# Kernel optimization log

Measured on AMD Instinct MI355X. Metric: run time of the kernel, lower is better.

Reference implementation:

```python
import jax, jax.numpy as jnp
import numpy as np

N, D, K, P, A = 16384, 256, 32, 64, 5
H, KD, NPT, FACT = 8, 32, 8, 2
RBF_BINS, RBF_MAX, REL_CLIP = 16, 10.0, 32


def _norm(v, eps=1e-6):
    return v * jax.lax.rsqrt(jnp.square(v).sum(-1, keepdims=True) + eps)


def extract_frames(pos):
    # pos: [N, A, 3]; backbone atoms 0=N, 1=CA, 2=C (Gram-Schmidt AF-style frame)
    n, ca, c = pos[:, 0], pos[:, 1], pos[:, 2]
    e1 = _norm(c - ca)
    u = n - ca
    e2 = _norm(u - (u * e1).sum(-1, keepdims=True) * e1)
    e3 = jnp.cross(e1, e2)
    R = jnp.stack([e1, e2, e3], axis=-1)  # [N,3,3], columns = frame axes
    t = ca
    local = jnp.einsum('nji,naj->nai', R, pos - t[:, None])  # R^T (p - t)
    return R, t, local


def distance_rbf(d):
    centers = jnp.linspace(0.0, RBF_MAX, RBF_BINS)
    sigma = RBF_MAX / RBF_BINS
    return jnp.exp(-jnp.square((d[..., None] - centers) / sigma))


def layer_norm(x, scale, offset, eps=1e-5):
    mu = x.mean(-1, keepdims=True)
    var = jnp.square(x - mu).mean(-1, keepdims=True)
    return (x - mu) * jax.lax.rsqrt(var + eps) * scale + offset


def setup_inputs() -> dict:
    key = jax.random.key(0)
    ks = jax.random.split(key, 20)
    f32 = jnp.float32
    rnd = lambda i, shape, s=0.02: jax.random.normal(ks[i], shape, f32) * s
    inp = {}
    inp['local'] = jax.random.normal(ks[0], (N, D), f32)
    inp['pos'] = jax.random.normal(ks[1], (N, A, 3), f32) * 3.0
    inp['neighbours'] = jax.random.randint(ks[2], (N, K), 0, N, jnp.int32)
    inp['resi'] = jnp.arange(N, dtype=jnp.int32) % 512
    inp['chain'] = jnp.arange(N, dtype=jnp.int32) // 2048
    inp['batch'] = jnp.arange(N, dtype=jnp.int32) // 4096
    inp['update_mask'] = jnp.ones((N, 1), bool)
    inp['mask'] = jnp.ones((N,), bool)
    FIN = A * 3 + A * RBF_BINS
    FPAIR = A * 3 + A * RBF_BINS + (2 * REL_CLIP + 1) + 2
    FOUT = H * KD + H * P + H * NPT * 3 + H * NPT
    inp['w_in'] = rnd(3, (FIN, D))
    inp['w_pair'] = rnd(4, (FPAIR, P))
    inp['b_pair'] = jnp.zeros((P,), f32)
    inp['ln1_s'] = jnp.ones((D,), f32); inp['ln1_o'] = jnp.zeros((D,), f32)
    inp['wq'] = rnd(5, (D, H * KD)); inp['wk'] = rnd(6, (D, H * KD)); inp['wv'] = rnd(7, (D, H * KD))
    inp['wqp'] = rnd(8, (D, H * NPT * 3)); inp['wkp'] = rnd(9, (D, H * NPT * 3)); inp['wvp'] = rnd(10, (D, H * NPT * 3))
    inp['wb'] = rnd(11, (P, H))
    inp['gamma'] = jnp.ones((H,), f32)
    inp['wo'] = rnd(12, (FOUT, D)); inp['bo'] = jnp.zeros((D,), f32)
    inp['ln2_s'] = jnp.ones((D,), f32); inp['ln2_o'] = jnp.zeros((D,), f32)
    DH = D * FACT
    inp['wg'] = rnd(13, (D, DH)); inp['wvm'] = rnd(14, (D, DH)); inp['wom'] = rnd(15, (DH, D))
    inp['ln3_s'] = jnp.ones((D,), f32); inp['ln3_o'] = jnp.zeros((D,), f32)
    inp['wpos'] = rnd(16, (D, A * 3))
    return inp


def reference(local, pos, w_in, w_pair, b_pair, ln1_s, ln1_o, wq, wk, wv, wqp, wkp, wvp,
              wb, gamma, wo, bo, ln2_s, ln2_o, wg, wvm, wom, ln3_s, ln3_o, wpos,
              neighbours, resi, chain, batch, update_mask, mask):
    n_res = local.shape[0]
    kk = neighbours.shape[1]
    R, t, local_pos = extract_frames(pos)  # [N,3,3], [N,3], [N,A,3]
    # --- geometric input features ---
    dloc = jnp.sqrt(jnp.square(local_pos).sum(-1) + 1e-12)
    feat = jnp.concatenate([_norm(local_pos).reshape(n_res, -1),
                            distance_rbf(dloc).reshape(n_res, -1)], axis=-1)
    local = local + feat @ w_in
    # --- pair features over kNN edges ---
    idx = jnp.clip(neighbours, 0, n_res - 1)
    pos_j = pos[idx]  # [N,K,A,3]
    rel = jnp.einsum('nji,nkaj->nkai', R, pos_j - t[:, None, None])  # neighbour atoms in frame i
    dij = jnp.sqrt(jnp.square(rel).sum(-1) + 1e-12)  # [N,K,A]
    dirs = rel / (dij[..., None] + 1e-6)
    rp = jnp.clip(resi[idx] - resi[:, None], -REL_CLIP, REL_CLIP) + REL_CLIP
    rp_oh = jax.nn.one_hot(rp, 2 * REL_CLIP + 1, dtype=local.dtype)
    same_chain = (chain[idx] == chain[:, None])[..., None].astype(local.dtype)
    same_batch = (batch[idx] == batch[:, None])[..., None].astype(local.dtype)
    pf = jnp.concatenate([dirs.reshape(n_res, kk, -1), distance_rbf(dij).reshape(n_res, kk, -1),
                          rp_oh, same_chain, same_batch], axis=-1)
    pair = jax.nn.gelu(pf @ w_pair + b_pair)  # [N,K,P]
    pair_mask = mask[:, None] & mask[idx] & (neighbours >= 0) & (batch[idx] == batch[:, None])
    # --- sparse invariant point attention ---
    x = layer_norm(local, ln1_s, ln1_o)
    q = (x @ wq).reshape(n_res, H, KD)
    k = (x @ wk).reshape(n_res, H, KD)
    v = (x @ wv).reshape(n_res, H, KD)
    to_glob = lambda pts: jnp.einsum('nij,nhpj->nhpi', R, pts) + t[:, None, None]
    qp = to_glob((x @ wqp).reshape(n_res, H, NPT, 3))
    kp = to_glob((x @ wkp).reshape(n_res, H, NPT, 3))
    vp = to_glob((x @ wvp).reshape(n_res, H, NPT, 3))
    qk = jnp.einsum('nhd,nkhd->nkh', q, k[idx]) / np.float32(np.sqrt(KD))
    d2 = jnp.square(qp[:, None] - kp[idx]).sum(-1).sum(-1)  # [N,K,H]
    wc = np.float32(np.sqrt(2.0 / (9.0 * NPT)))
    wl = np.float32(np.sqrt(1.0 / 3.0))
    logits = wl * (qk + pair @ wb - 0.5 * wc * jax.nn.softplus(gamma) * d2)
    logits = jnp.where(pair_mask[..., None], logits, -1e9)
    att = jax.nn.softmax(logits, axis=1)
    att = jnp.where(pair_mask[..., None], att, 0.0)
    o_s = jnp.einsum('nkh,nkhd->nhd', att, v[idx]).reshape(n_res, -1)
    o_pt = jnp.einsum('nkh,nkhpi->nhpi', att, vp[idx])
    o_pt = jnp.einsum('nji,nhpj->nhpi', R, o_pt - t[:, None, None])  # back to local frame
    o_n = jnp.sqrt(jnp.square(o_pt).sum(-1) + 1e-8)
    o_pr = jnp.einsum('nkh,nkc->nhc', att, pair).reshape(n_res, -1)
    ipa = jnp.concatenate([o_s, o_pr, o_pt.reshape(n_res, -1), o_n.reshape(n_res, -1)], -1) @ wo + bo
    local = local + ipa
    # --- gated MLP ---
    x = layer_norm(local, ln2_s, ln2_o)
    local = local + (jax.nn.gelu(x @ wg) * (x @ wvm)) @ wom
    # --- equivariant position update (scale = 1.0) ---
    x = layer_norm(local, ln3_s, ln3_o)
    new_lp = local_pos + (x @ wpos).reshape(n_res, A, 3)
    new_pos = jnp.einsum('nij,naj->nai', R, new_lp) + t[:, None]
    pos = jnp.where(update_mask[..., None], new_pos, pos)
    return local, pos
```

## Files before the change

### kernel.cpp

```cpp
#include <hip/hip_runtime.h>
#include <hip/hip_bf16.h>
#include <math.h>

#define DMODEL 256
#define KNB 32
#define NHEAD 8
#define FIN 95
#define FPD 95
#define KPAD 104
#define FOUT 1024
#define DHID 512
#define BTS 36
#define PRS 72

typedef __hip_bfloat16 bf16;
typedef __attribute__((ext_vector_type(8))) short short8;
typedef __attribute__((ext_vector_type(4))) float floatx4;

__device__ inline float B2F(bf16 x) { return __bfloat162float(x); }
__device__ inline bf16 F2B(float x) { return __float2bfloat16(x); }
__device__ inline unsigned short f2bs(float x) {
    bf16 h = __float2bfloat16(x);
    return *reinterpret_cast<unsigned short*>(&h);
}
__device__ inline float bs2f(short s) {
    return __uint_as_float(((unsigned)(unsigned short)s) << 16);
}

__device__ inline float gelu_f(float x) {
    float u = 1.5957691216057308f * x * (1.f + 0.044715f * x * x);
    float t = 1.f - 2.f / (1.f + __expf(u));
    return 0.5f * x * (1.f + t);
}

#define OFF_WALL 0
#define OFF_WO   344064
#define OFF_WG   606208
#define OFF_WVM  737280
#define OFF_WOM  868352
#define OFF_WP   999424
#define OFF_WIN  1006080
#define OFF_WBM  1032704
#define WT_TOTAL 1033728

__global__ __launch_bounds__(256) void kT(const float* __restrict__ wq, const float* __restrict__ wk,
                                          const float* __restrict__ wv, const float* __restrict__ wqp,
                                          const float* __restrict__ wkp, const float* __restrict__ wvp,
                                          const float* __restrict__ wo, const float* __restrict__ wg,
                                          const float* __restrict__ wvm, const float* __restrict__ wom,
                                          const float* __restrict__ w_pair, const float* __restrict__ w_in,
                                          const float* __restrict__ wbm,
                                          unsigned short* __restrict__ wt) {
    int stride = gridDim.x * 256;
    for (int e = blockIdx.x * 256 + threadIdx.x; e < WT_TOTAL; e += stride) {
        float v;
        if (e < OFF_WO) {
            int n = e >> 8, k = e & 255;
            if (n < 256) v = wq[k * 256 + n];
            else if (n < 512) v = wk[k * 256 + n - 256];
            else if (n < 768) v = wv[k * 256 + n - 512];
            else if (n < 960) v = wqp[k * 192 + n - 768];
            else if (n < 1152) v = wkp[k * 192 + n - 960];
            else v = wvp[k * 192 + n - 1152];
        } else if (e < OFF_WG) {
            int u = e - OFF_WO; int n = u >> 10, k = u & 1023;
            v = wo[k * 256 + n];
        } else if (e < OFF_WVM) {
            int u = e - OFF_WG; int n = u >> 8, k = u & 255;
            v = wg[k * 512 + n];
        } else if (e < OFF_WOM) {
            int u = e - OFF_WVM; int n = u >> 8, k = u & 255;
            v = wvm[k * 512 + n];
        } else if (e < OFF_WP) {
            int u = e - OFF_WOM; int n = u >> 9, k = u & 511;
            v = wom[k * 256 + n];
        } else if (e < OFF_WIN) {
            int u = e - OFF_WP; int n = u / KPAD, k = u % KPAD;
            v = (k < FPD) ? w_pair[k * 64 + n] : 0.f;
        } else if (e < OFF_WBM) {
            int u = e - OFF_WIN; int n = u / KPAD, k = u % KPAD;
            v = (k < FIN) ? w_in[k * 256 + n] : 0.f;
        } else {
            int u = e - OFF_WBM; int n = u >> 6, k = u & 63;
            v = (n < NHEAD) ? wbm[k * 8 + n] : 0.f;
        }
        wt[e] = f2bs(v);
    }
}

__global__ __launch_bounds__(256) void kA1(const float* __restrict__ pos,
                                           float* __restrict__ Rw,
                                           float* __restrict__ lpw,
                                           unsigned short* __restrict__ featb) {
    int tid = threadIdx.x;
    int res = tid >> 5, lt = tid & 31;
    int ri = blockIdx.x * 8 + res;
    const float* pp = pos + (size_t)ri * 15;
    float nx = pp[0], ny = pp[1], nz = pp[2];
    float cax = pp[3], cay = pp[4], caz = pp[5];
    float cx = pp[6], cy = pp[7], cz = pp[8];
    float e1x = cx - cax, e1y = cy - cay, e1z = cz - caz;
    float inv = rsqrtf(e1x * e1x + e1y * e1y + e1z * e1z + 1e-6f);
    e1x *= inv; e1y *= inv; e1z *= inv;
    float ux = nx - cax, uy = ny - cay, uz = nz - caz;
    float d = ux * e1x + uy * e1y + uz * e1z;
    float wx = ux - d * e1x, wy = uy - d * e1y, wz = uz - d * e1z;
    inv = rsqrtf(wx * wx + wy * wy + wz * wz + 1e-6f);
    float e2x = wx * inv, e2y = wy * inv, e2z = wz * inv;
    float e3x = e1y * e2z - e1z * e2y;
    float e3y = e1z * e2x - e1x * e2z;
    float e3z = e1x * e2y - e1y * e2x;
    float R[9] = {e1x, e2x, e3x, e1y, e2y, e3y, e1z, e2z, e3z};

    __shared__ float lpS[8][15];
    __shared__ float ddS[8][5], dinvS[8][5];

    if (lt < 9) Rw[(size_t)ri * 9 + lt] = R[lt];
    if (lt < 15) {
        int a = lt / 3, ii = lt % 3;
        float px = pp[a * 3 + 0] - cax, py = pp[a * 3 + 1] - cay, pz = pp[a * 3 + 2] - caz;
        float v = R[0 * 3 + ii] * px + R[1 * 3 + ii] * py + R[2 * 3 + ii] * pz;
        lpS[res][lt] = v;
        lpw[(size_t)ri * 15 + lt] = v;
    }
    __syncthreads();
    if (lt < 5) {
        float s = lpS[res][lt * 3] * lpS[res][lt * 3] + lpS[res][lt * 3 + 1] * lpS[res][lt * 3 + 1] +
                  lpS[res][lt * 3 + 2] * lpS[res][lt * 3 + 2];
        ddS[res][lt] = sqrtf(s + 1e-12f);
        dinvS[res][lt] = rsqrtf(s + 1e-6f);
    }
    __syncthreads();
    for (int e = lt; e < KPAD; e += 32) {
        float v;
        if (e < 15) v = lpS[res][e] * dinvS[res][e / 3];
        else if (e < 95) {
            int u = e - 15, a = u >> 4, b = u & 15;
            float z = (ddS[res][a] - (float)b * (10.f / 15.f)) * (1.f / 0.625f);
            v = __expf(-z * z);
        } else v = 0.f;
        featb[(size_t)ri * KPAD + e] = f2bs(v);
    }
}

__global__ __launch_bounds__(256) void kB(const float* __restrict__ local,
                                          const unsigned short* __restrict__ featb,
                                          const float* __restrict__ ln1_s,
                                          const float* __restrict__ ln1_o,
                                          const unsigned short* __restrict__ wAllT,
                                          const unsigned short* __restrict__ w_inT,
                                          float* __restrict__ dlocal,
                                          bf16* __restrict__ qbh, bf16* __restrict__ kvb,
                                          bf16* __restrict__ qpl, bf16* __restrict__ kpl,
                                          bf16* __restrict__ vpl) {
    int r0 = blockIdx.x * 32;
    int tid = threadIdx.x;
    __shared__ __align__(16) unsigned short featA[32 * KPAD];
    __shared__ __align__(16) unsigned short xbf[32 * 264];
    __shared__ float statsS[32 * 4];

    {
        const short8* src = reinterpret_cast<const short8*>(featb + (size_t)r0 * KPAD);
        short8* dst = reinterpret_cast<short8*>(featA);
        for (int c = tid; c < 32 * KPAD / 8; c += 256) dst[c] = src[c];
    }
    __syncthreads();

    int lane = tid & 63, w = tid >> 6;
    int mtile = w & 1, par = w >> 1;
    int m = lane & 15, quad = lane >> 4;

    short8 fa[3];
#pragma unroll
    for (int ks = 0; ks < 3; ks++)
        fa[ks] = *reinterpret_cast<const short8*>(&featA[(mtile * 16 + m) * KPAD + ks * 32 + quad * 8]);
    float lupv[8][4];
#pragma unroll
    for (int j = 0; j < 8; j++) {
        int nt = par + 2 * j;
        floatx4 c = {0.f, 0.f, 0.f, 0.f};
        const short8* bp = reinterpret_cast<const short8*>(w_inT + (size_t)(nt * 16 + m) * KPAD);
#pragma unroll
        for (int ks = 0; ks < 3; ks++)
            c = __builtin_amdgcn_mfma_f32_16x16x32_bf16(fa[ks], bp[ks * 4 + quad], c, 0, 0, 0);
        int col = nt * 16 + m;
#pragma unroll
        for (int r = 0; r < 4; r++) {
            int row = mtile * 16 + quad * 4 + r;
            float lv = local[(size_t)(r0 + row) * 256 + col] + c[r];
            lupv[j][r] = lv;
            dlocal[(size_t)(r0 + row) * 256 + col] = lv;
        }
    }
    {
        float s[4] = {0.f, 0.f, 0.f, 0.f}, ss[4] = {0.f, 0.f, 0.f, 0.f};
#pragma unroll
        for (int j = 0; j < 8; j++)
#pragma unroll
            for (int r = 0; r < 4; r++) { s[r] += lupv[j][r]; ss[r] += lupv[j][r] * lupv[j][r]; }
#pragma unroll
        for (int mask = 1; mask < 16; mask <<= 1)
#pragma unroll
            for (int r = 0; r < 4; r++) { s[r] += __shfl_xor(s[r], mask); ss[r] += __shfl_xor(ss[r], mask); }
        if (m == 0) {
#pragma unroll
            for (int r = 0; r < 4; r++) {
                int row = mtile * 16 + quad * 4 + r;
                statsS[row * 4 + par * 2 + 0] = s[r];
                statsS[row * 4 + par * 2 + 1] = ss[r];
            }
        }
    }
    __syncthreads();
    {
        float mu[4], rs_[4];
#pragma unroll
        for (int r = 0; r < 4; r++) {
            int row = mtile * 16 + quad * 4 + r;
            float S = statsS[row * 4 + 0] + statsS[row * 4 + 2];
            float SS = statsS[row * 4 + 1] + statsS[row * 4 + 3];
            float m_ = S * (1.f / 256.f);
            mu[r] = m_;
            rs_[r] = rsqrtf(SS * (1.f / 256.f) - m_ * m_ + 1e-5f);
        }
#pragma unroll
        for (int j = 0; j < 8; j++) {
            int col = (par + 2 * j) * 16 + m;
            float g = ln1_s[col], o = ln1_o[col];
#pragma unroll
            for (int r = 0; r < 4; r++) {
                int row = mtile * 16 + quad * 4 + r;
                xbf[row * 264 + col] = f2bs((lupv[j][r] - mu[r]) * rs_[r] * g + o);
            }
        }
    }
    __syncthreads();

    short8 afr[8];
#pragma unroll
    for (int ks = 0; ks < 8; ks++)
        afr[ks] = *reinterpret_cast<const short8*>(&xbf[(mtile * 16 + m) * 264 + ks * 32 + quad * 8]);
    for (int nt = par; nt < 84; nt += 2) {
        floatx4 c = {0.f, 0.f, 0.f, 0.f};
        const short8* bp = reinterpret_cast<const short8*>(wAllT + (size_t)(nt * 16 + m) * 256);
#pragma unroll
        for (int ks = 0; ks < 8; ks++)
            c = __builtin_amdgcn_mfma_f32_16x16x32_bf16(afr[ks], bp[ks * 4 + quad], c, 0, 0, 0);
        int colg = nt * 16 + m;
        bf16* O; int c0, ncol;
        if (colg < 256)       { O = qbh; c0 = colg;        ncol = 256; }
        else if (colg < 768)  { O = kvb; c0 = colg - 256;  ncol = 512; }
        else if (colg < 960)  { O = qpl; c0 = colg - 768;  ncol = 192; }
        else if (colg < 1152) { O = kpl; c0 = colg - 960;  ncol = 192; }
        else                  { O = vpl; c0 = colg - 1152; ncol = 192; }
#pragma unroll
        for (int r = 0; r < 4; r++) {
            int rg = r0 + mtile * 16 + quad * 4 + r;
            O[(size_t)rg * ncol + c0] = F2B(c[r]);
        }
    }
}

__global__ __launch_bounds__(256) void kP(const bf16* __restrict__ qpl,
                                          const bf16* __restrict__ kpl,
                                          const bf16* __restrict__ vpl,
                                          const float* __restrict__ Rw,
                                          const float* __restrict__ pos,
                                          float* __restrict__ qpg,
                                          bf16* __restrict__ kvpgh) {
    int r0 = blockIdx.x * 4;
    int tid = threadIdx.x;
    for (int u = tid; u < 4 * 192; u += 256) {
        int r = u / 192, e = u % 192, hp = e / 3, ii = e % 3;
        int ri = r0 + r;
        float R0 = Rw[(size_t)ri * 9 + ii * 3 + 0];
        float R1 = Rw[(size_t)ri * 9 + ii * 3 + 1];
        float R2 = Rw[(size_t)ri * 9 + ii * 3 + 2];
        float tt = pos[(size_t)ri * 15 + 3 + ii];
        size_t base = (size_t)ri * 192 + hp * 3;
        qpg[(size_t)ri * 192 + e] = R0 * B2F(qpl[base]) + R1 * B2F(qpl[base + 1]) + R2 * B2F(qpl[base + 2]) + tt;
        kvpgh[(size_t)ri * 384 + e] = F2B(R0 * B2F(kpl[base]) + R1 * B2F(kpl[base + 1]) + R2 * B2F(kpl[base + 2]));
        kvpgh[(size_t)ri * 384 + 192 + e] = F2B(R0 * B2F(vpl[base]) + R1 * B2F(vpl[base + 1]) + R2 * B2F(vpl[base + 2]));
    }
}

__global__ __launch_bounds__(256) void kC(const float* __restrict__ pos,
                                          const int* __restrict__ nbr,
                                          const int* __restrict__ resi,
                                          const int* __restrict__ chain,
                                          const int* __restrict__ batch,
                                          const int* __restrict__ mask,
                                          const float* __restrict__ Rw,
                                          const float* __restrict__ w_pair,
                                          const unsigned short* __restrict__ wT,
                                          const float* __restrict__ b_pair,
                                          const unsigned short* __restrict__ wbmT,
                                          const float* __restrict__ gamma,
                                          const bf16* __restrict__ qbh,
                                          const bf16* __restrict__ kvb,
                                          const float* __restrict__ qpg,
                                          const bf16* __restrict__ kvpgh,
                                          bf16* __restrict__ ipab,
                                          int N) {
    int i = blockIdx.x;
    int tid = threadIdx.x;
    __shared__ __align__(16) unsigned short BigT[512 * BTS];
    __shared__ __align__(16) unsigned short pairR[32 * PRS];
    __shared__ __align__(16) unsigned short attb[16 * 40];
    __shared__ __align__(16) float qS[256];
    __shared__ __align__(16) float qpS[192];
    __shared__ __align__(16) float pbS[256];
    __shared__ float spS[NHEAD];
    __shared__ float tjS[KNB][3];
    __shared__ float attjS[24];
    __shared__ int idxS[KNB], rpS[KNB], scS[KNB], sbS[KNB], pmS[KNB];
    __shared__ __align__(16) union UShare {
        unsigned short pfA[32 * KPAD];
        struct { float ipaS[FOUT]; float optg[192]; } o;
    } uS;

    int kk_s = tid & 31, seg = tid >> 5;
    int jpre;
    {
        int nb = nbr[(size_t)i * KNB + kk_s];
        jpre = min(max(nb, 0), N - 1);
    }
    short8 pv0, pv1, pv2, pv3, pp0, pp1, pp2;
    {
        const short8* vsrc = reinterpret_cast<const short8*>(kvb + (size_t)jpre * 512 + 256 + seg * 32);
        pv0 = vsrc[0]; pv1 = vsrc[1]; pv2 = vsrc[2]; pv3 = vsrc[3];
        const unsigned short* vpb = reinterpret_cast<const unsigned short*>(kvpgh) + (size_t)jpre * 384 + 192 + seg * 24;
        const short8* vpsrc = reinterpret_cast<const short8*>(vpb);
        pp0 = vpsrc[0]; pp1 = vpsrc[1]; pp2 = vpsrc[2];
    }

    float R[9];
#pragma unroll
    for (int u = 0; u < 9; u++) R[u] = Rw[(size_t)i * 9 + u];
    float t0 = pos[(size_t)i * 15 + 3];
    float t1 = pos[(size_t)i * 15 + 4];
    float t2 = pos[(size_t)i * 15 + 5];

    qS[tid] = B2F(qbh[(size_t)i * 256 + tid]);
    if (tid < 192) qpS[tid] = qpg[(size_t)i * 192 + tid];
    if (tid < NHEAD) spS[tid] = log1pf(__expf(gamma[tid]));
    if (tid < KNB) {
        int nb = nbr[(size_t)i * KNB + tid];
        int j = min(max(nb, 0), N - 1);
        idxS[tid] = j;
        int rp = resi[j] - resi[i];
        rp = min(max(rp, -32), 32) + 32;
        rpS[tid] = rp;
        scS[tid] = (chain[j] == chain[i]) ? 1 : 0;
        sbS[tid] = (batch[j] == batch[i]) ? 1 : 0;
        pmS[tid] = (mask[i] != 0 && mask[j] != 0 && nb >= 0 && batch[j] == batch[i]) ? 1 : 0;
    }
    __syncthreads();
    if (tid < 160) {
        int kk = tid & 31, a = tid >> 5;
        int j = idxS[kk];
        const float* pj = pos + (size_t)j * 15 + a * 3;
        float pj0 = pj[0], pj1 = pj[1], pj2 = pj[2];
        if (a == 1) { tjS[kk][0] = pj0; tjS[kk][1] = pj1; tjS[kk][2] = pj2; }
        float px = pj0 - t0, py = pj1 - t1, pz = pj2 - t2;
        float r0_ = R[0] * px + R[3] * py + R[6] * pz;
        float r1_ = R[1] * px + R[4] * py + R[7] * pz;
        float r2_ = R[2] * px + R[5] * py + R[8] * pz;
        float s = r0_ * r0_ + r1_ * r1_ + r2_ * r2_;
        float dij = sqrtf(s + 1e-12f);
        float di = 1.f / (dij + 1e-6f);
        uS.pfA[kk * KPAD + a * 3 + 0] = f2bs(r0_ * di);
        uS.pfA[kk * KPAD + a * 3 + 1] = f2bs(r1_ * di);
        uS.pfA[kk * KPAD + a * 3 + 2] = f2bs(r2_ * di);
        for (int b = 0; b < 16; b++) {
            float z = (dij - (float)b * (10.f / 15.f)) * (1.f / 0.625f);
            uS.pfA[kk * KPAD + 15 + a * 16 + b] = f2bs(__expf(-z * z));
        }
    }
    if (tid < KNB) uS.pfA[tid * KPAD + FPD] = 0;
    __syncthreads();

    {
        int lane = tid & 63;
        int wv = tid >> 6;
        int n0 = wv * 16;
        int mrow = lane & 15;
        int quad = lane >> 4;
        floatx4 c0 = {0.f, 0.f, 0.f, 0.f};
        floatx4 c1 = {0.f, 0.f, 0.f, 0.f};
#pragma unroll
        for (int ks = 0; ks < 3; ks++) {
            int k0 = ks * 32 + quad * 8;
            short8 a0 = *reinterpret_cast<const short8*>(&uS.pfA[mrow * KPAD + k0]);
            short8 a1 = *reinterpret_cast<const short8*>(&uS.pfA[(16 + mrow) * KPAD + k0]);
            short8 bb = *reinterpret_cast<const short8*>(&wT[(n0 + mrow) * KPAD + k0]);
            c0 = __builtin_amdgcn_mfma_f32_16x16x32_bf16(a0, bb, c0, 0, 0, 0);
            c1 = __builtin_amdgcn_mfma_f32_16x16x32_bf16(a1, bb, c1, 0, 0, 0);
        }
        int col = n0 + mrow;
        float bp = b_pair[col];
        float w160 = w_pair[160 * 64 + col];
        float w161 = w_pair[161 * 64 + col];
#pragma unroll
        for (int mt = 0; mt < 2; mt++) {
            floatx4 cc = mt ? c1 : c0;
#pragma unroll
            for (int r = 0; r < 4; r++) {
                int row = mt * 16 + quad * 4 + r;
                float s = cc[r] + bp + w_pair[(95 + rpS[row]) * 64 + col] +
                          (scS[row] ? w160 : 0.f) + (sbS[row] ? w161 : 0.f);
                unsigned short gb = f2bs(gelu_f(s));
                pairR[row * PRS + col] = gb;
                BigT[(448 + col) * BTS + row] = gb;
            }
        }
    }
    __syncthreads();

    short8 pk0, pk1, pk2, pk3, pq0, pq1, pq2;
    {
        int kk2 = tid >> 3, h2 = tid & 7;
        int j2 = idxS[kk2];
        const short8* ksrc = reinterpret_cast<const short8*>(kvb + (size_t)j2 * 512 + h2 * 32);
        pk0 = ksrc[0]; pk1 = ksrc[1]; pk2 = ksrc[2]; pk3 = ksrc[3];
        const unsigned short* kpb = reinterpret_cast<const unsigned short*>(kvpgh) + (size_t)j2 * 384 + h2 * 24;
        const short8* kpsrc = reinterpret_cast<const short8*>(kpb);
        pq0 = kpsrc[0]; pq1 = kpsrc[1]; pq2 = kpsrc[2];
    }
    {
        int kk = kk_s;
#pragma unroll
        for (int c = 0; c < 8; c++) BigT[(seg * 32 + c) * BTS + kk] = (unsigned short)pv0[c];
#pragma unroll
        for (int c = 0; c < 8; c++) BigT[(seg * 32 + 8 + c) * BTS + kk] = (unsigned short)pv1[c];
#pragma unroll
        for (int c = 0; c < 8; c++) BigT[(seg * 32 + 16 + c) * BTS + kk] = (unsigned short)pv2[c];
#pragma unroll
        for (int c = 0; c < 8; c++) BigT[(seg * 32 + 24 + c) * BTS + kk] = (unsigned short)pv3[c];
#pragma unroll
        for (int c = 0; c < 8; c++) BigT[(256 + seg * 24 + c) * BTS + kk] = (unsigned short)pp0[c];
#pragma unroll
        for (int c = 0; c < 8; c++) BigT[(256 + seg * 24 + 8 + c) * BTS + kk] = (unsigned short)pp1[c];
#pragma unroll
        for (int c = 0; c < 8; c++) BigT[(256 + seg * 24 + 16 + c) * BTS + kk] = (unsigned short)pp2[c];
    }
    {
        int w = tid >> 6;
        if (w < 2) {
            int lane = tid & 63, la = lane & 15, quad = lane >> 4;
            floatx4 c = {0.f, 0.f, 0.f, 0.f};
#pragma unroll
            for (int ks = 0; ks < 2; ks++) {
                short8 a = *reinterpret_cast<const short8*>(&pairR[(w * 16 + la) * PRS + ks * 32 + quad * 8]);
                short8 b = *reinterpret_cast<const short8*>(wbmT + la * 64 + ks * 32 + quad * 8);
                c = __builtin_amdgcn_mfma_f32_16x16x32_bf16(a, b, c, 0, 0, 0);
            }
            if (la < NHEAD) {
#pragma unroll
                for (int r = 0; r < 4; r++)
                    pbS[(w * 16 + quad * 4 + r) * 8 + la] = c[r];
            }
        }
    }
    __syncthreads();

    {
        int kk = tid >> 3, h = tid & 7;
        float qk = 0.f;
        const floatx4* qh4 = reinterpret_cast<const floatx4*>(qS + h * 32);
        short8 kvv[4] = {pk0, pk1, pk2, pk3};
#pragma unroll
        for (int e = 0; e < 4; e++) {
            short8 kv = kvv[e];
            floatx4 qa = qh4[2 * e], qb = qh4[2 * e + 1];
            qk += qa[0] * bs2f(kv[0]) + qa[1] * bs2f(kv[1]) + qa[2] * bs2f(kv[2]) + qa[3] * bs2f(kv[3]) +
                  qb[0] * bs2f(kv[4]) + qb[1] * bs2f(kv[5]) + qb[2] * bs2f(kv[6]) + qb[3] * bs2f(kv[7]);
        }
        qk *= 0.17677669529663687f;
        float d2 = 0.f;
        const float* qp = qpS + h * 24;
        float tj[3] = {tjS[kk][0], tjS[kk][1], tjS[kk][2]};
        short8 kpv[3] = {pq0, pq1, pq2};
#pragma unroll
        for (int e8 = 0; e8 < 3; e8++)
#pragma unroll
            for (int c8 = 0; c8 < 8; c8++) {
                int x = e8 * 8 + c8;
                float df = (qp[x] - tj[x % 3]) - bs2f(kpv[e8][c8]);
                d2 += df * df;
            }
        float pb = pbS[kk * 8 + h];
        float lgt = 0.5773502691896258f * (qk + pb - (1.f / 12.f) * spS[h] * d2);
        pbS[kk * 8 + h] = pmS[kk] ? lgt : -1e9f;
    }
    __syncthreads();

    if (tid < 64) {
        int h = tid >> 3, sub = tid & 7;
        float m = -INFINITY;
        float lv[4];
#pragma unroll
        for (int q = 0; q < 4; q++) {
            lv[q] = pbS[(sub + 8 * q) * 8 + h];
            m = fmaxf(m, lv[q]);
        }
#pragma unroll
        for (int mk = 1; mk < 8; mk <<= 1) m = fmaxf(m, __shfl_xor(m, mk));
        float s = 0.f, ex[4];
#pragma unroll
        for (int q = 0; q < 4; q++) { ex[q] = __expf(lv[q] - m); s += ex[q]; }
#pragma unroll
        for (int mk = 1; mk < 8; mk <<= 1) s += __shfl_xor(s, mk);
        float invs = 1.f / s;
#pragma unroll
        for (int q = 0; q < 4; q++) {
            int kk = sub + 8 * q;
            float a = pmS[kk] ? ex[q] * invs : 0.f;
            attb[h * 40 + kk] = f2bs(a);
            pbS[kk * 8 + h] = a;
        }
    } else if (tid < 128) {
        int t2 = tid - 64;
        int h2 = 8 + (t2 >> 3);
        int k0 = (t2 & 7) * 4;
#pragma unroll
        for (int q = 0; q < 4; q++) attb[h2 * 40 + k0 + q] = 0;
    }
    __syncthreads();

    {
        int lane = tid & 63, w = tid >> 6;
        int la = lane & 15, quad = lane >> 4;
        short8 af = *reinterpret_cast<const short8*>(&attb[la * 40 + quad * 8]);
        float* oB = uS.o.ipaS;
#pragma unroll
        for (int n8 = 0; n8 < 8; n8++) {
            int nt = w * 8 + n8;
            int colg = nt * 16 + la;
            union { short8 s; unsigned long long u[2]; } bb;
            const unsigned long long* bp = reinterpret_cast<const unsigned long long*>(&BigT[colg * BTS + quad * 8]);
            bb.u[0] = bp[0]; bb.u[1] = bp[1];
            floatx4 z = {0.f, 0.f, 0.f, 0.f};
            floatx4 d = __builtin_amdgcn_mfma_f32_16x16x32_bf16(af, bb.s, z, 0, 0, 0);
            if (quad < 2) {
                if (colg < 448) {
                    int h_req, dst;
                    if (colg < 256) { h_req = colg >> 5; dst = (h_req << 5) + (colg & 31); }
                    else            { int e = colg - 256; h_req = e / 24; dst = 1024 + e; }
                    if ((h_req >> 2) == quad) {
#pragma unroll
                        for (int r = 0; r < 4; r++)
                            if ((h_req & 3) == r) oB[dst] = d[r];
                    }
                } else {
                    int c = colg - 448;
#pragma unroll
                    for (int r = 0; r < 4; r++)
                        oB[256 + (quad * 4 + r) * 64 + c] = d[r];
                }
            }
        }
    }
    if (tid < 24) {
        int h = tid / 3, c = tid % 3;
        float s = 0.f;
#pragma unroll
        for (int kk = 0; kk < KNB; kk++) s += pbS[kk * 8 + h] * tjS[kk][c];
        attjS[tid] = s;
    }
    __syncthreads();

    if (tid < 192) {
        int hp = tid / 3, ii = tid % 3;
        int h = hp >> 3;
        const float* optg = uS.o.ipaS + 1024;
        float v0 = optg[hp * 3 + 0] + attjS[h * 3 + 0] - t0;
        float v1 = optg[hp * 3 + 1] + attjS[h * 3 + 1] - t1;
        float v2 = optg[hp * 3 + 2] + attjS[h * 3 + 2] - t2;
        uS.o.ipaS[768 + tid] = R[0 + ii] * v0 + R[3 + ii] * v1 + R[6 + ii] * v2;
    }
    __syncthreads();
    if (tid < 64) {
        float a0 = uS.o.ipaS[768 + tid * 3], a1 = uS.o.ipaS[768 + tid * 3 + 1], a2 = uS.o.ipaS[768 + tid * 3 + 2];
        uS.o.ipaS[960 + tid] = sqrtf(a0 * a0 + a1 * a1 + a2 * a2 + 1e-8f);
    }
    __syncthreads();
    for (int u = tid; u < FOUT; u += 256) ipab[(size_t)i * FOUT + u] = F2B(uS.o.ipaS[u]);
}

__global__ __launch_bounds__(256) void kDE(const bf16* __restrict__ ipab,
                                           const unsigned short* __restrict__ woT,
                                           const float* __restrict__ bo,
                                           const float* __restrict__ ln2_s,
                                           const float* __restrict__ ln2_o,
                                           const unsigned short* __restrict__ wgT,
                                           const unsigned short* __restrict__ wvmT,
                                           const unsigned short* __restrict__ womT,
                                           float* __restrict__ dlocal) {
    int r0 = blockIdx.x * 32;
    int tid = threadIdx.x;
    __shared__ __align__(16) unsigned short xbf[32 * 264];
    __shared__ __align__(16) unsigned short hbf[32 * 520];
    __shared__ float statsS[32 * 4];
    int lane = tid & 63, w = tid >> 6;
    int mtile = w & 1, par = w >> 1, m = lane & 15, quad = lane >> 4;

    floatx4 l2[8];
#pragma unroll
    for (int j = 0; j < 8; j++) l2[j] = {0.f, 0.f, 0.f, 0.f};
    const short8* arow = reinterpret_cast<const short8*>(ipab + (size_t)(r0 + mtile * 16 + m) * 1024);
    for (int ks = 0; ks < 32; ks++) {
        short8 a = arow[ks * 4 + quad];
#pragma unroll
        for (int j = 0; j < 8; j++) {
            int nt = par + 2 * j;
            const short8* bp = reinterpret_cast<const short8*>(woT + (size_t)(nt * 16 + m) * 1024);
            l2[j] = __builtin_amdgcn_mfma_f32_16x16x32_bf16(a, bp[ks * 4 + quad], l2[j], 0, 0, 0);
        }
    }
#pragma unroll
    for (int j = 0; j < 8; j++) {
        int colg = (par + 2 * j) * 16 + m;
        float bov = bo[colg];
#pragma unroll
        for (int r = 0; r < 4; r++) {
            int row = mtile * 16 + quad * 4 + r;
            l2[j][r] += dlocal[(size_t)(r0 + row) * 256 + colg] + bov;
        }
    }
    {
        float s[4] = {0.f, 0.f, 0.f, 0.f}, ss[4] = {0.f, 0.f, 0.f, 0.f};
#pragma unroll
        for (int j = 0; j < 8; j++)
#pragma unroll
            for (int r = 0; r < 4; r++) { s[r] += l2[j][r]; ss[r] += l2[j][r] * l2[j][r]; }
#pragma unroll
        for (int mask = 1; mask < 16; mask <<= 1)
#pragma unroll
            for (int r = 0; r < 4; r++) { s[r] += __shfl_xor(s[r], mask); ss[r] += __shfl_xor(ss[r], mask); }
        if (m == 0) {
#pragma unroll
            for (int r = 0; r < 4; r++) {
                int row = mtile * 16 + quad * 4 + r;
                statsS[row * 4 + par * 2 + 0] = s[r];
                statsS[row * 4 + par * 2 + 1] = ss[r];
            }
        }
    }
    __syncthreads();
    {
        float mu[4], rs_[4];
#pragma unroll
        for (int r = 0; r < 4; r++) {
            int row = mtile * 16 + quad * 4 + r;
            float S = statsS[row * 4 + 0] + statsS[row * 4 + 2];
            float SS = statsS[row * 4 + 1] + statsS[row * 4 + 3];
            float m_ = S * (1.f / 256.f);
            mu[r] = m_;
            rs_[r] = rsqrtf(SS * (1.f / 256.f) - m_ * m_ + 1e-5f);
        }
#pragma unroll
        for (int j = 0; j < 8; j++) {
            int colg = (par + 2 * j) * 16 + m;
            float g = ln2_s[colg], o = ln2_o[colg];
#pragma unroll
            for (int r = 0; r < 4; r++) {
                int row = mtile * 16 + quad * 4 + r;
                xbf[row * 264 + colg] = f2bs((l2[j][r] - mu[r]) * rs_[r] * g + o);
            }
        }
    }
    __syncthreads();
    short8 afr[8];
#pragma unroll
    for (int ks = 0; ks < 8; ks++)
        afr[ks] = *reinterpret_cast<const short8*>(&xbf[(mtile * 16 + m) * 264 + ks * 32 + quad * 8]);
    for (int nt = par; nt < 32; nt += 2) {
        floatx4 cg = {0.f, 0.f, 0.f, 0.f};
        floatx4 cv = {0.f, 0.f, 0.f, 0.f};
        const short8* bg = reinterpret_cast<const short8*>(wgT + (size_t)(nt * 16 + m) * 256);
        const short8* bv = reinterpret_cast<const short8*>(wvmT + (size_t)(nt * 16 + m) * 256);
#pragma unroll
        for (int ks = 0; ks < 8; ks++) {
            cg = __builtin_amdgcn_mfma_f32_16x16x32_bf16(afr[ks], bg[ks * 4 + quad], cg, 0, 0, 0);
            cv = __builtin_amdgcn_mfma_f32_16x16x32_bf16(afr[ks], bv[ks * 4 + quad], cv, 0, 0, 0);
        }
#pragma unroll
        for (int r = 0; r < 4; r++) {
            int row = mtile * 16 + quad * 4 + r;
            hbf[row * 520 + nt * 16 + m] = f2bs(gelu_f(cg[r]) * cv[r]);
        }
    }
    __syncthreads();
    floatx4 acc[8];
#pragma unroll
    for (int j = 0; j < 8; j++) acc[j] = {0.f, 0.f, 0.f, 0.f};
    for (int ks = 0; ks < 16; ks++) {
        short8 a = *reinterpret_cast<const short8*>(&hbf[(mtile * 16 + m) * 520 + ks * 32 + quad * 8]);
#pragma unroll
        for (int j = 0; j < 8; j++) {
            int nt = par + 2 * j;
            const short8* bp = reinterpret_cast<const short8*>(womT + (size_t)(nt * 16 + m) * 512);
            acc[j] = __builtin_amdgcn_mfma_f32_16x16x32_bf16(a, bp[ks * 4 + quad], acc[j], 0, 0, 0);
        }
    }
#pragma unroll
    for (int j = 0; j < 8; j++) {
        int colg = (par + 2 * j) * 16 + m;
#pragma unroll
        for (int r = 0; r < 4; r++) {
            int row = mtile * 16 + quad * 4 + r;
            dlocal[(size_t)(r0 + row) * 256 + colg] = l2[j][r] + acc[j][r];
        }
    }
}

__global__ __launch_bounds__(256) void kF(const float* __restrict__ dlocal,
                                          const float* __restrict__ ln3_s,
                                          const float* __restrict__ ln3_o,
                                          const float* __restrict__ wpos,
                                          const float* __restrict__ lpw,
                                          const float* __restrict__ Rw,
                                          const float* __restrict__ pos,
                                          const int* __restrict__ umask,
                                          float* __restrict__ outp) {
    int tid = threadIdx.x;
    int r = tid >> 5, lt = tid & 31;
    int ri = blockIdx.x * 8 + r;
    __shared__ float x3S[8][256];
    __shared__ float nlS[8][15];
    {
        const floatx4* src = reinterpret_cast<const floatx4*>(dlocal + (size_t)ri * 256 + lt * 8);
        floatx4 v0 = src[0], v1 = src[1];
        float s = 0.f, ss = 0.f;
#pragma unroll
        for (int q = 0; q < 4; q++) {
            s += v0[q] + v1[q];
            ss += v0[q] * v0[q] + v1[q] * v1[q];
        }
#pragma unroll
        for (int mask = 1; mask < 32; mask <<= 1) { s += __shfl_xor(s, mask); ss += __shfl_xor(ss, mask); }
        float mu = s * (1.f / 256.f);
        float var = ss * (1.f / 256.f) - mu * mu;
        float rs = rsqrtf(var + 1e-5f);
#pragma unroll
        for (int q = 0; q < 4; q++) {
            int f0 = lt * 8 + q, f1 = lt * 8 + 4 + q;
            x3S[r][f0] = (v0[q] - mu) * rs * ln3_s[f0] + ln3_o[f0];
            x3S[r][f1] = (v1[q] - mu) * rs * ln3_s[f1] + ln3_o[f1];
        }
    }
    __syncthreads();
    {
        int g = tid >> 5, sub = tid & 31;
        for (int out = g; out < 120; out += 8) {
            int rr = out / 15, e = out % 15;
            float partial = 0.f;
#pragma unroll
            for (int i2 = 0; i2 < 8; i2++) {
                int f = sub + 32 * i2;
                partial += x3S[rr][f] * wpos[f * 15 + e];
            }
#pragma unroll
            for (int mask = 1; mask < 32; mask <<= 1) partial += __shfl_xor(partial, mask);
            if (sub == 0) nlS[rr][e] = lpw[(size_t)(blockIdx.x * 8 + rr) * 15 + e] + partial;
        }
    }
    __syncthreads();
    if (tid < 120) {
        int rr = tid / 15, e = tid % 15;
        int rj = blockIdx.x * 8 + rr;
        int a2 = e / 3, ii = e % 3;
        float R0 = Rw[(size_t)rj * 9 + ii * 3 + 0];
        float R1 = Rw[(size_t)rj * 9 + ii * 3 + 1];
        float R2 = Rw[(size_t)rj * 9 + ii * 3 + 2];
        float tt = pos[(size_t)rj * 15 + 3 + ii];
        float np = R0 * nlS[rr][a2 * 3 + 0] + R1 * nlS[rr][a2 * 3 + 1] + R2 * nlS[rr][a2 * 3 + 2] + tt;
        float old = pos[(size_t)rj * 15 + e];
        outp[(size_t)rj * 15 + e] = (umask[rj] != 0) ? np : old;
    }
}

extern "C" void kernel_launch(void* const* d_in, const int* in_sizes, int n_in,
                              void* d_out, int out_size, void* d_ws, size_t ws_size,
                              hipStream_t stream) {
    static const int map_dict[31] = {0, 1, 2, 3, 4, 5, 6, 7, 8, 9, 10, 11, 12, 13, 14, 15,
                                     16, 17, 18, 19, 20, 21, 22, 23, 24, 25, 26, 27, 28, 29, 30};
    static const int map_sig[31] = {0, 1, 25, 26, 27, 28, 29, 30, 2, 3, 4, 5, 6, 7, 8, 9,
                                    10, 11, 12, 13, 14, 15, 16, 17, 18, 19, 20, 21, 22, 23, 24};
    const int* M = (in_sizes[2] == FIN * DMODEL) ? map_sig : map_dict;

    const float* local = (const float*)d_in[M[0]];
    const float* pos = (const float*)d_in[M[1]];
    const int* nbr = (const int*)d_in[M[2]];
    const int* resi = (const int*)d_in[M[3]];
    const int* chain = (const int*)d_in[M[4]];
    const int* batch = (const int*)d_in[M[5]];
    const int* umask = (const int*)d_in[M[6]];
    const int* mask = (const int*)d_in[M[7]];
    const float* w_in = (const float*)d_in[M[8]];
    const float* w_pair = (const float*)d_in[M[9]];
    const float* b_pair = (const float*)d_in[M[10]];
    const float* ln1_s = (const float*)d_in[M[11]];
    const float* ln1_o = (const float*)d_in[M[12]];
    const float* wq = (const float*)d_in[M[13]];
    const float* wk = (const float*)d_in[M[14]];
    const float* wv = (const float*)d_in[M[15]];
    const float* wqp = (const float*)d_in[M[16]];
    const float* wkp = (const float*)d_in[M[17]];
    const float* wvp = (const float*)d_in[M[18]];
    const float* wbm = (const float*)d_in[M[19]];
    const float* gamma = (const float*)d_in[M[20]];
    const float* wo = (const float*)d_in[M[21]];
    const float* bo = (const float*)d_in[M[22]];
    const float* ln2_s = (const float*)d_in[M[23]];
    const float* ln2_o = (const float*)d_in[M[24]];
    const float* wg = (const float*)d_in[M[25]];
    const float* wvm = (const float*)d_in[M[26]];
    const float* wom = (const float*)d_in[M[27]];
    const float* ln3_s = (const float*)d_in[M[28]];
    const float* ln3_o = (const float*)d_in[M[29]];
    const float* wpos = (const float*)d_in[M[30]];

    int N = in_sizes[0] / DMODEL;

    float* out_local = (float*)d_out;
    float* out_pos = out_local + (size_t)N * DMODEL;

    char* wsb = (char*)d_ws;
    float* Rw = (float*)wsb;   wsb += (size_t)N * 9 * 4;
    float* lpw = (float*)wsb;  wsb += (size_t)N * 15 * 4;
    bf16* qbh = (bf16*)wsb;    wsb += (size_t)N * 256 * 2;
    bf16* kvb = (bf16*)wsb;    wsb += (size_t)N * 512 * 2;
    bf16* qpl = (bf16*)wsb;    wsb += (size_t)N * 192 * 2;
    bf16* kpl = (bf16*)wsb;    wsb += (size_t)N * 192 * 2;
    bf16* vpl = (bf16*)wsb;    wsb += (size_t)N * 192 * 2;
    bf16* ipab = (bf16*)wsb;   wsb += (size_t)N * 1024 * 2;
    float* qpg = (float*)wsb;  wsb += (size_t)N * 192 * 4;
    bf16* kvpgh = (bf16*)wsb;  wsb += (size_t)N * 384 * 2;
    unsigned short* featb = (unsigned short*)wsb; wsb += (size_t)N * KPAD * 2;
    unsigned short* wtrans = (unsigned short*)wsb; wsb += (size_t)WT_TOTAL * 2;
    unsigned short* wAllT = wtrans + OFF_WALL;
    unsigned short* woT   = wtrans + OFF_WO;
    unsigned short* wgT   = wtrans + OFF_WG;
    unsigned short* wvmT  = wtrans + OFF_WVM;
    unsigned short* womT  = wtrans + OFF_WOM;
    unsigned short* wpT   = wtrans + OFF_WP;
    unsigned short* winT  = wtrans + OFF_WIN;
    unsigned short* wbmT  = wtrans + OFF_WBM;

    dim3 blk(256);
    hipLaunchKernelGGL(kT, dim3(512), blk, 0, stream, wq, wk, wv, wqp, wkp, wvp,
                       wo, wg, wvm, wom, w_pair, w_in, wbm, wtrans);
    hipLaunchKernelGGL(kA1, dim3(N / 8), blk, 0, stream, pos, Rw, lpw, featb);
    hipLaunchKernelGGL(kB, dim3(N / 32), blk, 0, stream, local, featb, ln1_s, ln1_o, wAllT, winT,
                       out_local, qbh, kvb, qpl, kpl, vpl);
    hipLaunchKernelGGL(kP, dim3(N / 4), blk, 0, stream, qpl, kpl, vpl, Rw, pos, qpg, kvpgh);
    hipLaunchKernelGGL(kC, dim3(N), blk, 0, stream, pos, nbr, resi, chain, batch, mask, Rw,
                       w_pair, wpT, b_pair, wbmT, gamma, qbh, kvb, qpg, kvpgh, ipab, N);
    hipLaunchKernelGGL(kDE, dim3(N / 32), blk, 0, stream, ipab, woT, bo, ln2_s, ln2_o,
                       wgT, wvmT, womT, out_local);
    hipLaunchKernelGGL(kF, dim3(N / 8), blk, 0, stream, out_local, ln3_s, ln3_o, wpos, lpw, Rw, pos,
                       umask, out_pos);
}
```

Measured before the change: 680.1 us.

## Halve BigT shared buffer by splitting attention-weighted MFMA into two passes

Cuts the transposed neighbour-value staging buffer in half in shared memory. The V columns are processed first, then the buffer is refilled with the value points and a transposed copy of the pair features for a second MFMA pass. It also sets launch_bounds(256, 4) so more blocks can be resident per CU. The cost is an extra __syncthreads, an extra copy of pairR into BigT, and register pressure from the occupancy hint, in exchange for lower LDS use.

```diff
diff --git a/kernel.cpp b/kernel.cpp
--- a/kernel.cpp
+++ b/kernel.cpp
@@ -284,7 +284,7 @@
     }
 }
 
-__global__ __launch_bounds__(256) void kC(const float* __restrict__ pos,
+__global__ __launch_bounds__(256, 4) void kC(const float* __restrict__ pos,
                                           const int* __restrict__ nbr,
                                           const int* __restrict__ resi,
                                           const int* __restrict__ chain,
@@ -304,7 +304,7 @@
                                           int N) {
     int i = blockIdx.x;
     int tid = threadIdx.x;
-    __shared__ __align__(16) unsigned short BigT[512 * BTS];
+    __shared__ __align__(16) unsigned short BigT[256 * BTS];
     __shared__ __align__(16) unsigned short pairR[32 * PRS];
     __shared__ __align__(16) unsigned short attb[16 * 40];
     __shared__ __align__(16) float qS[256];
@@ -409,9 +409,7 @@
                 int row = mt * 16 + quad * 4 + r;
                 float s = cc[r] + bp + w_pair[(95 + rpS[row]) * 64 + col] +
                           (scS[row] ? w160 : 0.f) + (sbS[row] ? w161 : 0.f);
-                unsigned short gb = f2bs(gelu_f(s));
-                pairR[row * PRS + col] = gb;
-                BigT[(448 + col) * BTS + row] = gb;
+                pairR[row * PRS + col] = f2bs(gelu_f(s));
             }
         }
     }
@@ -437,12 +435,6 @@
         for (int c = 0; c < 8; c++) BigT[(seg * 32 + 16 + c) * BTS + kk] = (unsigned short)pv2[c];
 #pragma unroll
         for (int c = 0; c < 8; c++) BigT[(seg * 32 + 24 + c) * BTS + kk] = (unsigned short)pv3[c];
-#pragma unroll
-        for (int c = 0; c < 8; c++) BigT[(256 + seg * 24 + c) * BTS + kk] = (unsigned short)pp0[c];
-#pragma unroll
-        for (int c = 0; c < 8; c++) BigT[(256 + seg * 24 + 8 + c) * BTS + kk] = (unsigned short)pp1[c];
-#pragma unroll
-        for (int c = 0; c < 8; c++) BigT[(256 + seg * 24 + 16 + c) * BTS + kk] = (unsigned short)pp2[c];
     }
     {
         int w = tid >> 6;
@@ -528,37 +520,23 @@
     }
     __syncthreads();
 
-    {
-        int lane = tid & 63, w = tid >> 6;
-        int la = lane & 15, quad = lane >> 4;
-        short8 af = *reinterpret_cast<const short8*>(&attb[la * 40 + quad * 8]);
-        float* oB = uS.o.ipaS;
-#pragma unroll
-        for (int n8 = 0; n8 < 8; n8++) {
-            int nt = w * 8 + n8;
-            int colg = nt * 16 + la;
-            union { short8 s; unsigned long long u[2]; } bb;
-            const unsigned long long* bp = reinterpret_cast<const unsigned long long*>(&BigT[colg * BTS + quad * 8]);
-            bb.u[0] = bp[0]; bb.u[1] = bp[1];
-            floatx4 z = {0.f, 0.f, 0.f, 0.f};
-            floatx4 d = __builtin_amdgcn_mfma_f32_16x16x32_bf16(af, bb.s, z, 0, 0, 0);
-            if (quad < 2) {
-                if (colg < 448) {
-                    int h_req, dst;
-                    if (colg < 256) { h_req = colg >> 5; dst = (h_req << 5) + (colg & 31); }
-                    else            { int e = colg - 256; h_req = e / 24; dst = 1024 + e; }
-                    if ((h_req >> 2) == quad) {
-#pragma unroll
-                        for (int r = 0; r < 4; r++)
-                            if ((h_req & 3) == r) oB[dst] = d[r];
-                    }
-                } else {
-                    int c = colg - 448;
-#pragma unroll
-                    for (int r = 0; r < 4; r++)
-                        oB[256 + (quad * 4 + r) * 64 + c] = d[r];
-                }
-            }
+    int la_ = (tid & 63) & 15, quad_ = (tid & 63) >> 4, w_ = tid >> 6;
+    short8 af = *reinterpret_cast<const short8*>(&attb[la_ * 40 + quad_ * 8]);
+    float* oB = uS.o.ipaS;
+
+#pragma unroll
+    for (int n4 = 0; n4 < 4; n4++) {
+        int colg = (w_ * 4 + n4) * 16 + la_;
+        union { short8 s; unsigned long long u[2]; } bb;
+        const unsigned long long* bp = reinterpret_cast<const unsigned long long*>(&BigT[colg * BTS + quad_ * 8]);
+        bb.u[0] = bp[0]; bb.u[1] = bp[1];
+        floatx4 z = {0.f, 0.f, 0.f, 0.f};
+        floatx4 d = __builtin_amdgcn_mfma_f32_16x16x32_bf16(af, bb.s, z, 0, 0, 0);
+        int h_req = colg >> 5;
+        if (quad_ == (h_req >> 2)) {
+#pragma unroll
+            for (int r = 0; r < 4; r++)
+                if ((h_req & 3) == r) oB[(h_req << 5) + (colg & 31)] = d[r];
         }
     }
     if (tid < 24) {
@@ -567,6 +545,47 @@
 #pragma unroll
         for (int kk = 0; kk < KNB; kk++) s += pbS[kk * 8 + h] * tjS[kk][c];
         attjS[tid] = s;
+    }
+    __syncthreads();
+
+    {
+        int kk = kk_s;
+#pragma unroll
+        for (int c = 0; c < 8; c++) BigT[(seg * 24 + c) * BTS + kk] = (unsigned short)pp0[c];
+#pragma unroll
+        for (int c = 0; c < 8; c++) BigT[(seg * 24 + 8 + c) * BTS + kk] = (unsigned short)pp1[c];
+#pragma unroll
+        for (int c = 0; c < 8; c++) BigT[(seg * 24 + 16 + c) * BTS + kk] = (unsigned short)pp2[c];
+    }
+#pragma unroll
+    for (int q = 0; q < 8; q++) {
+        int u = tid + q * 256;
+        int row = u & 31, col = u >> 5;
+        BigT[(192 + col) * BTS + row] = pairR[row * PRS + col];
+    }
+    __syncthreads();
+
+#pragma unroll
+    for (int n4 = 0; n4 < 4; n4++) {
+        int colg = (w_ * 4 + n4) * 16 + la_;
+        union { short8 s; unsigned long long u[2]; } bb;
+        const unsigned long long* bp = reinterpret_cast<const unsigned long long*>(&BigT[colg * BTS + quad_ * 8]);
+        bb.u[0] = bp[0]; bb.u[1] = bp[1];
+        floatx4 z = {0.f, 0.f, 0.f, 0.f};
+        floatx4 d = __builtin_amdgcn_mfma_f32_16x16x32_bf16(af, bb.s, z, 0, 0, 0);
+        if (colg < 192) {
+            int h_req = colg / 24;
+            if (quad_ == (h_req >> 2)) {
+#pragma unroll
+                for (int r = 0; r < 4; r++)
+                    if ((h_req & 3) == r) oB[1024 + colg] = d[r];
+            }
+        } else if (quad_ < 2) {
+            int c = colg - 192;
+#pragma unroll
+            for (int r = 0; r < 4; r++)
+                oB[256 + (quad_ * 4 + r) * 64 + c] = d[r];
+        }
     }
     __syncthreads();
 
```

Measured after the change: 638.8 us. 6.1% less time.
